# Kernel tuning notes

Hardware: AMD Instinct MI355X
Metric: run time of the kernel (lower is better)

The kernel has to match this reference:

```python
import jax, jax.numpy as jnp
import numpy as np

NEG_SLOPE = 0.2

def edge_softmax(logits, dst, num_nodes):
    # logits: [E, H]; softmax over incoming edges of each dst node, per head
    m = jax.ops.segment_max(logits, dst, num_segments=num_nodes)  # [N, H]
    e = jnp.exp(logits - m[dst])
    s = jax.ops.segment_sum(e, dst, num_segments=num_nodes)  # [N, H]
    return e / s[dst]

def gat_layer(h, src, dst, W, al, ar, b, activation):
    # W: [F_in, H*D], al/ar: [H, D], b: [H, D]
    N = h.shape[0]
    H, D = al.shape
    feat = (h @ W).reshape(N, H, D)
    el = jnp.sum(feat * al, axis=-1)  # [N, H]
    er = jnp.sum(feat * ar, axis=-1)  # [N, H]
    e = jax.nn.leaky_relu(el[src] + er[dst], NEG_SLOPE)  # [E, H]
    a = edge_softmax(e, dst, N)  # [E, H]
    msg = feat[src] * a[:, :, None]  # [E, H, D]
    rst = jax.ops.segment_sum(msg, dst, num_segments=N) + b[None]  # [N, H, D]
    if activation:
        rst = jax.nn.relu(rst)
    return rst

def setup_inputs() -> dict:
    key = jax.random.key(0)
    ks = jax.random.split(key, 16)
    N, E = 50000, 800000
    IN, HID, OUT, H = 128, 64, 64, 4
    s = 0.1
    return {
        "features": jax.random.normal(ks[0], (N, IN), jnp.float32),
        "src": jax.random.randint(ks[1], (E,), 0, N),
        "dst": jax.random.randint(ks[2], (E,), 0, N),
        "W1": jax.random.normal(ks[3], (IN, H * HID), jnp.float32) * s,
        "al1": jax.random.normal(ks[4], (H, HID), jnp.float32) * s,
        "ar1": jax.random.normal(ks[5], (H, HID), jnp.float32) * s,
        "b1": jnp.zeros((H, HID), jnp.float32),
        "W2": jax.random.normal(ks[6], (H * HID, H * HID), jnp.float32) * s,
        "al2": jax.random.normal(ks[7], (H, HID), jnp.float32) * s,
        "ar2": jax.random.normal(ks[8], (H, HID), jnp.float32) * s,
        "b2": jnp.zeros((H, HID), jnp.float32),
        "W3": jax.random.normal(ks[9], (H * HID, OUT), jnp.float32) * s,
        "al3": jax.random.normal(ks[10], (1, OUT), jnp.float32) * s,
        "ar3": jax.random.normal(ks[11], (1, OUT), jnp.float32) * s,
        "b3": jnp.zeros((1, OUT), jnp.float32),
    }

def reference(features, src, dst, W1, al1, ar1, b1, W2, al2, ar2, b2, W3, al3, ar3, b3):
    N = features.shape[0]
    h = gat_layer(features, src, dst, W1, al1, ar1, b1, activation=True)   # [N, 4, 64]
    h = h.reshape(N, -1)                                                    # [N, 256]
    h = gat_layer(h, src, dst, W2, al2, ar2, b2, activation=True)          # [N, 4, 64]
    h = h.reshape(N, -1)                                                    # [N, 256]
    h = gat_layer(h, src, dst, W3, al3, ar3, b3, activation=False)         # [N, 1, 64]
    return h.mean(axis=1)                                                   # [N, 64]
```

## Files before the change

kernel.cpp:

```cpp
#include <hip/hip_runtime.h>
#include <hip/hip_bf16.h>

#define LEAKY 0.2f

typedef __attribute__((ext_vector_type(8))) short short8;
typedef __attribute__((ext_vector_type(4))) float f32x4;

__device__ inline unsigned short f2b(float f) {
    unsigned u = __float_as_uint(f);
    u += 0x7FFFu + ((u >> 16) & 1u);
    return (unsigned short)(u >> 16);
}
__device__ inline float b2f(unsigned short s) {
    return __uint_as_float(((unsigned)s) << 16);
}

#define NEB 8192


__global__ __launch_bounds__(256)
void k_prep(const float* __restrict__ features, unsigned short* __restrict__ fconv,
            int n4,
            const float* __restrict__ W1, const float* __restrict__ W2,
            const float* __restrict__ W3, unsigned short* __restrict__ Wt1,
            unsigned short* __restrict__ Wt2, unsigned short* __restrict__ Wt3,
            const int* __restrict__ dst, int* __restrict__ hist, int nbb,
            int E, int N) {
    __shared__ int lc[256];
    const int tid = threadIdx.x;
    if (blockIdx.x < nbb) {
        lc[tid] = 0;
        __syncthreads();
        const int b0 = blockIdx.x * NEB;
        const int cnt = min(NEB, E - b0);
        for (int j = 0; j < NEB / 256; ++j) {
            int idx = j * 256 + tid;
            if (idx < cnt) {
                int dn = dst[b0 + idx];
                if ((unsigned)dn < (unsigned)N) atomicAdd(&lc[dn >> 8], 1);
            }
        }
        __syncthreads();
        hist[blockIdx.x * 256 + tid] = lc[tid];
        return;
    }
    int idx = (blockIdx.x - nbb) * 256 + tid;
    if (idx < n4) {
        float4 v = *(const float4*)(features + idx * 4);
        ushort4 o;
        o.x = f2b(v.x); o.y = f2b(v.y); o.z = f2b(v.z); o.w = f2b(v.w);
        *(ushort4*)(fconv + idx * 4) = o;
        return;
    }
    int j = idx - n4;
    if (j < 32768) {
        int m = j >> 7, k = j & 127;
        Wt1[j] = f2b(W1[(size_t)k * 256 + m]);
        return;
    }
    if (j < 98304) {
        int jj = j - 32768;
        int m = jj >> 8, k = jj & 255;
        Wt2[jj] = f2b(W2[(size_t)k * 256 + m]);
        return;
    }
    if (j < 114688) {
        int jj = j - 98304;
        int m = jj >> 8, k = jj & 255;
        Wt3[jj] = f2b(W3[(size_t)k * 64 + m]);
    }
}


__global__ __launch_bounds__(256)
void k_bucket_scan(const int* __restrict__ hist, int nbb, int* __restrict__ bbase,
                   int* __restrict__ bcur, int* __restrict__ row_start_N, int B, int E) {
    __shared__ int ws[4];
    const int tid = threadIdx.x, lane = tid & 63, wave = tid >> 6;
    int v = 0;
    for (int blk = 0; blk < nbb; ++blk) v += hist[blk * 256 + tid];
    if (tid >= B) v = 0;
    int x = v;
    #pragma unroll
    for (int off = 1; off < 64; off <<= 1) {
        int t = __shfl_up(x, off, 64);
        if (lane >= off) x += t;
    }
    if (lane == 63) ws[wave] = x;
    __syncthreads();
    if (tid == 0) {
        int c = 0;
        #pragma unroll
        for (int wv = 0; wv < 4; ++wv) { int t = ws[wv]; ws[wv] = c; c += t; }
    }
    __syncthreads();
    int excl = x - v + ws[wave];
    if (tid < B) { bbase[tid] = excl; bcur[tid] = excl; }
    if (tid == 0) { bbase[B] = E; *row_start_N = E; }
}

__global__ __launch_bounds__(256)
void k_bin_scatter(const int* __restrict__ dst, int* __restrict__ bcur,
                   int* __restrict__ ebuf, int E, int N) {
    __shared__ int lc[256], lofs[256], lcur[256], gres[256];
    __shared__ int stage_e[NEB];
    __shared__ unsigned short stage_d[NEB];
    __shared__ int ws[4];
    const int tid = threadIdx.x, lane = tid & 63, wave = tid >> 6;
    const int b0 = blockIdx.x * NEB;
    const int cnt = min(NEB, E - b0);
    lc[tid] = 0;
    __syncthreads();

    int dreg[NEB / 256];
    #pragma unroll
    for (int j = 0; j < NEB / 256; ++j) {
        int idx = j * 256 + tid;
        dreg[j] = -1;
        if (idx < cnt) {
            int dn = dst[b0 + idx];
            if ((unsigned)dn < (unsigned)N) {
                dreg[j] = dn;
                atomicAdd(&lc[dn >> 8], 1);
            }
        }
    }
    __syncthreads();
    {
        int v = lc[tid];
        int x = v;
        #pragma unroll
        for (int off = 1; off < 64; off <<= 1) {
            int t = __shfl_up(x, off, 64);
            if (lane >= off) x += t;
        }
        if (lane == 63) ws[wave] = x;
        __syncthreads();
        if (tid == 0) {
            int c = 0;
            #pragma unroll
            for (int wv = 0; wv < 4; ++wv) { int t = ws[wv]; ws[wv] = c; c += t; }
        }
        __syncthreads();
        int excl = x - v + ws[wave];
        lofs[tid] = excl;
        lcur[tid] = excl;
    }
    __syncthreads();
    #pragma unroll
    for (int j = 0; j < NEB / 256; ++j) {
        int dn = dreg[j];
        if (dn >= 0) {
            int p = atomicAdd(&lcur[dn >> 8], 1);
            stage_e[p] = b0 + j * 256 + tid;
            stage_d[p] = (unsigned short)dn;
        }
    }
    __syncthreads();
    if (lc[tid] > 0) gres[tid] = atomicAdd(&bcur[tid], lc[tid]);
    __syncthreads();
    int total = lcur[255];
    for (int i = tid; i < total; i += 256) {
        int dn = stage_d[i];
        int k = dn >> 8;
        int dest = gres[k] + (i - lofs[k]);
        ebuf[dest] = ((dn & 255) << 24) | stage_e[i];
    }
}

__global__ __launch_bounds__(256)
void k_csr_build(const int* __restrict__ ebuf, const int* __restrict__ src,
                 const int* __restrict__ bbase, int* __restrict__ row_start,
                 int* __restrict__ src_sorted, int N) {
    __shared__ int lc[256], lcur[256];
    __shared__ int ws[4];
    const int tid = threadIdx.x, lane = tid & 63, wave = tid >> 6;
    const int k = blockIdx.x;
    const int base = k << 8;
    const int e0 = bbase[k];
    const int cnt = bbase[k + 1] - e0;
    lc[tid] = 0;
    __syncthreads();
    for (int i = tid; i < cnt; i += 256) {
        int rel = ((unsigned)ebuf[e0 + i]) >> 24;
        atomicAdd(&lc[rel], 1);
    }
    __syncthreads();
    {
        int v = lc[tid];
        int x = v;
        #pragma unroll
        for (int off = 1; off < 64; off <<= 1) {
            int t = __shfl_up(x, off, 64);
            if (lane >= off) x += t;
        }
        if (lane == 63) ws[wave] = x;
        __syncthreads();
        if (tid == 0) {
            int c = 0;
            #pragma unroll
            for (int wv = 0; wv < 4; ++wv) { int t = ws[wv]; ws[wv] = c; c += t; }
        }
        __syncthreads();
        int excl = x - v + ws[wave];
        lcur[tid] = excl;
        int n = base + tid;
        if (n < N) row_start[n] = e0 + excl;
    }
    __syncthreads();
    for (int i = tid; i < cnt; i += 256) {
        int val = ebuf[e0 + i];
        int rel = ((unsigned)val) >> 24;
        int e = val & 0xFFFFFF;
        int p = atomicAdd(&lcur[rel], 1);
        src_sorted[e0 + p] = src[e];
    }
}


__global__ __launch_bounds__(256)
void k_gemm_mfma(const unsigned short* __restrict__ A, const unsigned short* __restrict__ Wt,
                 unsigned short* __restrict__ Cb, const float* __restrict__ al,
                 const float* __restrict__ ar, float* __restrict__ el,
                 float* __restrict__ er, int N, int K, int M) {
    constexpr int STR = 40;
    __shared__ unsigned short As[128 * STR];
    __shared__ unsigned short Bs[128 * STR];
    const int tid  = threadIdx.x;
    const int wave = tid >> 6;
    const int lane = tid & 63;
    const int row0 = blockIdx.y * 128;
    const int col0 = blockIdx.x * 128;
    const int wr = (wave >> 1) * 64;
    const int wc = (wave & 1) * 64;
    const int m16 = lane & 15;
    const int q   = lane >> 4;

    const int s_row = tid >> 1;
    const int s_off = (tid & 1) * 16;

    f32x4 acc[4][4] = {};

    for (int k0 = 0; k0 < K; k0 += 32) {
        {
            int gr = row0 + s_row;
            short8 z = {};
            short8 v0 = z, v1 = z;
            if (gr < N) {
                const unsigned short* ap = A + (size_t)gr * K + k0 + s_off;
                v0 = *(const short8*)ap;
                v1 = *(const short8*)(ap + 8);
            }
            *(short8*)&As[s_row * STR + s_off]     = v0;
            *(short8*)&As[s_row * STR + s_off + 8] = v1;
        }
        {
            const unsigned short* sp = Wt + (size_t)(col0 + s_row) * K + k0 + s_off;
            *(short8*)&Bs[s_row * STR + s_off]     = *(const short8*)sp;
            *(short8*)&Bs[s_row * STR + s_off + 8] = *(const short8*)(sp + 8);
        }
        __syncthreads();

        short8 afr[4], bfr[4];
        #pragma unroll
        for (int rg = 0; rg < 4; ++rg)
            afr[rg] = *(const short8*)&As[(wr + rg * 16 + m16) * STR + q * 8];
        #pragma unroll
        for (int cg = 0; cg < 4; ++cg)
            bfr[cg] = *(const short8*)&Bs[(wc + cg * 16 + m16) * STR + q * 8];
        #pragma unroll
        for (int rg = 0; rg < 4; ++rg)
            #pragma unroll
            for (int cg = 0; cg < 4; ++cg)
                acc[rg][cg] = __builtin_amdgcn_mfma_f32_16x16x32_bf16(
                    afr[rg], bfr[cg], acc[rg][cg], 0, 0, 0);
        __syncthreads();
    }

    const int H = M >> 6;
    const int h = (col0 + wc) >> 6;
    float alv[4], arv[4];
    #pragma unroll
    for (int cg = 0; cg < 4; ++cg) {
        alv[cg] = al[h * 64 + cg * 16 + m16];
        arv[cg] = ar[h * 64 + cg * 16 + m16];
    }

    #pragma unroll
    for (int rg = 0; rg < 4; ++rg) {
        #pragma unroll
        for (int r = 0; r < 4; ++r) {
            int gr = row0 + wr + rg * 16 + q * 4 + r;
            float pl = 0.f, pr = 0.f;
            #pragma unroll
            for (int cg = 0; cg < 4; ++cg) {
                pl = fmaf(acc[rg][cg][r], alv[cg], pl);
                pr = fmaf(acc[rg][cg][r], arv[cg], pr);
            }
            #pragma unroll
            for (int off = 1; off < 16; off <<= 1) {
                pl += __shfl_xor(pl, off, 64);
                pr += __shfl_xor(pr, off, 64);
            }
            if (gr < N) {
                unsigned short* bp = Cb + (size_t)gr * M + col0 + wc + m16;
                #pragma unroll
                for (int cg = 0; cg < 4; ++cg)
                    bp[cg * 16] = f2b(acc[rg][cg][r]);
                if (m16 == 0) {
                    el[gr * H + h] = pl;
                    er[gr * H + h] = pr;
                }
            }
        }
    }
}


__global__ __launch_bounds__(256)
void k_gemm_mfma64(const unsigned short* __restrict__ A, const unsigned short* __restrict__ Wt,
                   unsigned short* __restrict__ Cb, const float* __restrict__ al,
                   const float* __restrict__ ar, float* __restrict__ el,
                   float* __restrict__ er, int N, int K) {
    constexpr int M = 64;
    constexpr int STR = 40;
    __shared__ unsigned short As[256 * STR];
    __shared__ unsigned short Bs[64 * STR];
    const int tid  = threadIdx.x;
    const int wave = tid >> 6;
    const int lane = tid & 63;
    const int row0 = blockIdx.x * 256;
    const int wr = wave * 64;
    const int m16 = lane & 15;
    const int q   = lane >> 4;

    const int s_row = tid >> 1;
    const int s_off = (tid & 1) * 16;
    const int b_row = tid >> 2;
    const int b_chk = (tid & 3) * 8;

    f32x4 acc[4][4] = {};

    for (int k0 = 0; k0 < K; k0 += 32) {
        #pragma unroll
        for (int p = 0; p < 2; ++p) {
            int r = s_row + p * 128;
            int gr = row0 + r;
            short8 z = {};
            short8 v0 = z, v1 = z;
            if (gr < N) {
                const unsigned short* ap = A + (size_t)gr * K + k0 + s_off;
                v0 = *(const short8*)ap;
                v1 = *(const short8*)(ap + 8);
            }
            *(short8*)&As[r * STR + s_off]     = v0;
            *(short8*)&As[r * STR + s_off + 8] = v1;
        }
        {
            const unsigned short* sp = Wt + (size_t)b_row * K + k0 + b_chk;
            *(short8*)&Bs[b_row * STR + b_chk] = *(const short8*)sp;
        }
        __syncthreads();

        short8 afr[4], bfr[4];
        #pragma unroll
        for (int rg = 0; rg < 4; ++rg)
            afr[rg] = *(const short8*)&As[(wr + rg * 16 + m16) * STR + q * 8];
        #pragma unroll
        for (int cg = 0; cg < 4; ++cg)
            bfr[cg] = *(const short8*)&Bs[(cg * 16 + m16) * STR + q * 8];
        #pragma unroll
        for (int rg = 0; rg < 4; ++rg)
            #pragma unroll
            for (int cg = 0; cg < 4; ++cg)
                acc[rg][cg] = __builtin_amdgcn_mfma_f32_16x16x32_bf16(
                    afr[rg], bfr[cg], acc[rg][cg], 0, 0, 0);
        __syncthreads();
    }

    float alv[4], arv[4];
    #pragma unroll
    for (int cg = 0; cg < 4; ++cg) {
        alv[cg] = al[cg * 16 + m16];
        arv[cg] = ar[cg * 16 + m16];
    }

    #pragma unroll
    for (int rg = 0; rg < 4; ++rg) {
        #pragma unroll
        for (int r = 0; r < 4; ++r) {
            int gr = row0 + wr + rg * 16 + q * 4 + r;
            float pl = 0.f, pr = 0.f;
            #pragma unroll
            for (int cg = 0; cg < 4; ++cg) {
                pl = fmaf(acc[rg][cg][r], alv[cg], pl);
                pr = fmaf(acc[rg][cg][r], arv[cg], pr);
            }
            #pragma unroll
            for (int off = 1; off < 16; off <<= 1) {
                pl += __shfl_xor(pl, off, 64);
                pr += __shfl_xor(pr, off, 64);
            }
            if (gr < N) {
                unsigned short* bp = Cb + (size_t)gr * M + m16;
                #pragma unroll
                for (int cg = 0; cg < 4; ++cg)
                    bp[cg * 16] = f2b(acc[rg][cg][r]);
                if (m16 == 0) {
                    el[gr] = pl;
                    er[gr] = pr;
                }
            }
        }
    }
}

template<int OUTBF>
__global__ __launch_bounds__(256)
void k_agg_f(const int* __restrict__ row_start, const int* __restrict__ src_sorted,
             const uint4* __restrict__ featp, const float* __restrict__ el,
             const float* __restrict__ er, const float* __restrict__ bias,
             void* __restrict__ outv, int H, int N, int do_relu) {
    const int M = H * 64;
    const int P = M >> 3;
    const int G = 256 / P;
    const int grp = threadIdx.x / P;
    const int t = threadIdx.x - grp * P;
    const int n = blockIdx.x * G + grp;
    if (n >= N) return;
    const int d0 = t * 8;
    const int h = d0 >> 6;
    const float erv = er[n * H + h];

    const int b0 = row_start[n], b1 = row_start[n + 1];

    float a[8] = {};
    float sum = 0.f;
    int i = b0;
    for (; i + 8 <= b1; i += 8) {
        int ss[8]; float wv[8]; uint4 pv[8];
        #pragma unroll
        for (int j = 0; j < 8; ++j) ss[j] = src_sorted[i + j];
        #pragma unroll
        for (int j = 0; j < 8; ++j) wv[j] = el[(size_t)ss[j] * H + h];
        #pragma unroll
        for (int j = 0; j < 8; ++j) pv[j] = featp[(size_t)ss[j] * P + t];
        #pragma unroll
        for (int j = 0; j < 8; ++j) {
            float x = wv[j] + erv;
            x = (x > 0.f) ? x : LEAKY * x;
            float w = __expf(x);
            wv[j] = w;
            sum += w;
        }
        #pragma unroll
        for (int j = 0; j < 8; ++j) {
            a[0] = fmaf(__uint_as_float(pv[j].x << 16),         wv[j], a[0]);
            a[1] = fmaf(__uint_as_float(pv[j].x & 0xFFFF0000u), wv[j], a[1]);
            a[2] = fmaf(__uint_as_float(pv[j].y << 16),         wv[j], a[2]);
            a[3] = fmaf(__uint_as_float(pv[j].y & 0xFFFF0000u), wv[j], a[3]);
            a[4] = fmaf(__uint_as_float(pv[j].z << 16),         wv[j], a[4]);
            a[5] = fmaf(__uint_as_float(pv[j].z & 0xFFFF0000u), wv[j], a[5]);
            a[6] = fmaf(__uint_as_float(pv[j].w << 16),         wv[j], a[6]);
            a[7] = fmaf(__uint_as_float(pv[j].w & 0xFFFF0000u), wv[j], a[7]);
        }
    }
    for (; i + 4 <= b1; i += 4) {
        int ss[4]; float wv[4]; uint4 pv[4];
        #pragma unroll
        for (int j = 0; j < 4; ++j) ss[j] = src_sorted[i + j];
        #pragma unroll
        for (int j = 0; j < 4; ++j) wv[j] = el[(size_t)ss[j] * H + h];
        #pragma unroll
        for (int j = 0; j < 4; ++j) pv[j] = featp[(size_t)ss[j] * P + t];
        #pragma unroll
        for (int j = 0; j < 4; ++j) {
            float x = wv[j] + erv;
            x = (x > 0.f) ? x : LEAKY * x;
            float w = __expf(x);
            wv[j] = w;
            sum += w;
        }
        #pragma unroll
        for (int j = 0; j < 4; ++j) {
            a[0] = fmaf(__uint_as_float(pv[j].x << 16),         wv[j], a[0]);
            a[1] = fmaf(__uint_as_float(pv[j].x & 0xFFFF0000u), wv[j], a[1]);
            a[2] = fmaf(__uint_as_float(pv[j].y << 16),         wv[j], a[2]);
            a[3] = fmaf(__uint_as_float(pv[j].y & 0xFFFF0000u), wv[j], a[3]);
            a[4] = fmaf(__uint_as_float(pv[j].z << 16),         wv[j], a[4]);
            a[5] = fmaf(__uint_as_float(pv[j].z & 0xFFFF0000u), wv[j], a[5]);
            a[6] = fmaf(__uint_as_float(pv[j].w << 16),         wv[j], a[6]);
            a[7] = fmaf(__uint_as_float(pv[j].w & 0xFFFF0000u), wv[j], a[7]);
        }
    }
    for (; i < b1; ++i) {
        int ss = src_sorted[i];
        float x = el[(size_t)ss * H + h] + erv;
        uint4 pv = featp[(size_t)ss * P + t];
        x = (x > 0.f) ? x : LEAKY * x;
        float w = __expf(x);
        sum += w;
        a[0] = fmaf(__uint_as_float(pv.x << 16),         w, a[0]);
        a[1] = fmaf(__uint_as_float(pv.x & 0xFFFF0000u), w, a[1]);
        a[2] = fmaf(__uint_as_float(pv.y << 16),         w, a[2]);
        a[3] = fmaf(__uint_as_float(pv.y & 0xFFFF0000u), w, a[3]);
        a[4] = fmaf(__uint_as_float(pv.z << 16),         w, a[4]);
        a[5] = fmaf(__uint_as_float(pv.z & 0xFFFF0000u), w, a[5]);
        a[6] = fmaf(__uint_as_float(pv.w << 16),         w, a[6]);
        a[7] = fmaf(__uint_as_float(pv.w & 0xFFFF0000u), w, a[7]);
    }

    float rs = 1.0f / fmaxf(sum, 1e-30f);
    float4 bv0 = *(const float4*)(bias + d0);
    float4 bv1 = *(const float4*)(bias + d0 + 4);
    a[0] = fmaf(a[0], rs, bv0.x); a[1] = fmaf(a[1], rs, bv0.y);
    a[2] = fmaf(a[2], rs, bv0.z); a[3] = fmaf(a[3], rs, bv0.w);
    a[4] = fmaf(a[4], rs, bv1.x); a[5] = fmaf(a[5], rs, bv1.y);
    a[6] = fmaf(a[6], rs, bv1.z); a[7] = fmaf(a[7], rs, bv1.w);
    if (do_relu) {
        #pragma unroll
        for (int j = 0; j < 8; ++j) a[j] = fmaxf(a[j], 0.f);
    }
    if (OUTBF) {
        uint4 o;
        o.x = (unsigned)f2b(a[0]) | ((unsigned)f2b(a[1]) << 16);
        o.y = (unsigned)f2b(a[2]) | ((unsigned)f2b(a[3]) << 16);
        o.z = (unsigned)f2b(a[4]) | ((unsigned)f2b(a[5]) << 16);
        o.w = (unsigned)f2b(a[6]) | ((unsigned)f2b(a[7]) << 16);
        *(uint4*)((unsigned short*)outv + (size_t)n * M + d0) = o;
    } else {
        *(float4*)((float*)outv + (size_t)n * M + d0)     = make_float4(a[0], a[1], a[2], a[3]);
        *(float4*)((float*)outv + (size_t)n * M + d0 + 4) = make_float4(a[4], a[5], a[6], a[7]);
    }
}


static void run_layer(const unsigned short* A, int K, const unsigned short* Wt,
                      const float* al_, const float* ar_, const float* b_, int H,
                      unsigned short* featb, void* rstOut, bool outBf,
                      float* el, float* er,
                      const int* row_start, const int* src_sorted,
                      int N, int E, bool do_relu, hipStream_t stream) {
    const int M = H * 64;
    if (M % 128 == 0) {
        dim3 gg(M / 128, (N + 127) / 128);
        k_gemm_mfma<<<gg, 256, 0, stream>>>(A, Wt, featb, al_, ar_, el, er, N, K, M);
    } else {
        k_gemm_mfma64<<<(N + 255) / 256, 256, 0, stream>>>(A, Wt, featb, al_, ar_, el, er, N, K);
    }

    int G = 256 / (M / 8);
    if (outBf)
        k_agg_f<1><<<(N + G - 1) / G, 256, 0, stream>>>(row_start, src_sorted,
                                                        (const uint4*)featb, el, er,
                                                        b_, rstOut, H, N, do_relu ? 1 : 0);
    else
        k_agg_f<0><<<(N + G - 1) / G, 256, 0, stream>>>(row_start, src_sorted,
                                                        (const uint4*)featb, el, er,
                                                        b_, rstOut, H, N, do_relu ? 1 : 0);
}

extern "C" void kernel_launch(void* const* d_in, const int* in_sizes, int n_in,
                              void* d_out, int out_size, void* d_ws, size_t ws_size,
                              hipStream_t stream) {
    const float* features = (const float*)d_in[0];
    const int*   src = (const int*)d_in[1];
    const int*   dst = (const int*)d_in[2];
    const float* W1  = (const float*)d_in[3];
    const float* al1 = (const float*)d_in[4];
    const float* ar1 = (const float*)d_in[5];
    const float* b1  = (const float*)d_in[6];
    const float* W2  = (const float*)d_in[7];
    const float* al2 = (const float*)d_in[8];
    const float* ar2 = (const float*)d_in[9];
    const float* b2  = (const float*)d_in[10];
    const float* W3  = (const float*)d_in[11];
    const float* al3 = (const float*)d_in[12];
    const float* ar3 = (const float*)d_in[13];
    const float* b3  = (const float*)d_in[14];

    const int N = in_sizes[0] / 128;
    const int E = in_sizes[1];
    const int B = (N + 255) >> 8;
    const int n4 = N * 128 / 4;
    const int nbb = (E + NEB - 1) / NEB;

    float* ws   = (float*)d_ws;
    float* el   = ws;
    float* er   = el + (size_t)N * 4;
    int* row_start  = (int*)(er + (size_t)N * 4);
    int* src_sorted = row_start + N + 1;
    int* ebuf       = src_sorted + E;
    int* bbase      = ebuf + E;
    int* bcur       = bbase + 257;
    int* hist       = bcur + 256;
    uintptr_t wp = (uintptr_t)(hist + (size_t)nbb * 256);
    wp = (wp + 15) & ~(uintptr_t)15;
    unsigned short* Wt1   = (unsigned short*)wp;
    unsigned short* Wt2   = Wt1 + 32768;
    unsigned short* Wt3   = Wt2 + 65536;
    unsigned short* fconv = Wt3 + 16384;
    unsigned short* featb = fconv + (size_t)N * 128;
    unsigned short* rstb  = featb + (size_t)N * 256;

    int prep_total = n4 + 114688;
    int prep_blocks = nbb + (prep_total + 255) / 256;
    k_prep<<<prep_blocks, 256, 0, stream>>>(features, fconv, n4,
                                            W1, W2, W3, Wt1, Wt2, Wt3,
                                            dst, hist, nbb, E, N);

    k_bucket_scan<<<1, 256, 0, stream>>>(hist, nbb, bbase, bcur, row_start + N, B, E);
    k_bin_scatter<<<nbb, 256, 0, stream>>>(dst, bcur, ebuf, E, N);
    k_csr_build<<<B, 256, 0, stream>>>(ebuf, src, bbase, row_start, src_sorted, N);

    run_layer(fconv, 128, Wt1, al1, ar1, b1, 4, featb, rstb, true,
              el, er, row_start, src_sorted, N, E, true, stream);
    run_layer(rstb, 256, Wt2, al2, ar2, b2, 4, featb, rstb, true,
              el, er, row_start, src_sorted, N, E, true, stream);
    run_layer(rstb, 256, Wt3, al3, ar3, b3, 1, featb, d_out, false,
              el, er, row_start, src_sorted, N, E, false, stream);
}
```

Measured before the change: 398.1 us.

## Double-buffer edge gathers in aggregation, use exp2 with pre-scaled logits, template head count

The aggregation kernel's main edge loop now software-pipelines batches of eight edges. It issues the next batch's index, logit and feature gathers before computing on the current batch, to hide gather latency. The GEMM epilogues pre-multiply el/er by log2(e) so the softmax weight can use the hardware exp2 instruction directly, and leaky-relu becomes a max. The head count is a template parameter and indices use 32-bit arithmetic, which cuts address math. Holding two buffers in flight raises register pressure and may reduce occupancy.

```diff
diff --git a/kernel.cpp b/kernel.cpp
--- a/kernel.cpp
+++ b/kernel.cpp
@@ -2,6 +2,7 @@
 #include <hip/hip_bf16.h>
 
 #define LEAKY 0.2f
+#define LOG2E 1.44269504f
 
 typedef __attribute__((ext_vector_type(8))) short short8;
 typedef __attribute__((ext_vector_type(4))) float f32x4;
@@ -14,6 +15,7 @@
 __device__ inline float b2f(unsigned short s) {
     return __uint_as_float(((unsigned)s) << 16);
 }
+__device__ inline float fexp2(float x) { return __builtin_amdgcn_exp2f(x); }
 
 #define NEB 8192
 
@@ -308,8 +310,8 @@
                 for (int cg = 0; cg < 4; ++cg)
                     bp[cg * 16] = f2b(acc[rg][cg][r]);
                 if (m16 == 0) {
-                    el[gr * H + h] = pl;
-                    er[gr * H + h] = pr;
+                    el[gr * H + h] = pl * LOG2E;
+                    er[gr * H + h] = pr * LOG2E;
                 }
             }
         }
@@ -407,77 +409,102 @@
                 for (int cg = 0; cg < 4; ++cg)
                     bp[cg * 16] = f2b(acc[rg][cg][r]);
                 if (m16 == 0) {
-                    el[gr] = pl;
-                    er[gr] = pr;
+                    el[gr] = pl * LOG2E;
+                    er[gr] = pr * LOG2E;
                 }
             }
         }
     }
 }
 
-template<int OUTBF>
+
+#define AGG_LOADB(SS, ELV, PV, BASE) do {                                     \
+    _Pragma("unroll") for (int j = 0; j < 8; ++j)                             \
+        SS[j] = src_sorted[(BASE) + j];                                       \
+    _Pragma("unroll") for (int j = 0; j < 8; ++j)                             \
+        ELV[j] = el[(unsigned)(SS[j] * HH + h)];                              \
+    _Pragma("unroll") for (int j = 0; j < 8; ++j)                             \
+        PV[j] = featp[(unsigned)(SS[j] * P + t)];                             \
+} while (0)
+
+#define AGG_COMPUTEB(ELV, PV) do {                                            \
+    float wvv[8];                                                             \
+    _Pragma("unroll") for (int j = 0; j < 8; ++j) {                           \
+        float x = ELV[j] + erv;                                               \
+        x = fmaxf(x, LEAKY * x);                                              \
+        float w = fexp2(x);                                                   \
+        wvv[j] = w; sum += w;                                                 \
+    }                                                                         \
+    _Pragma("unroll") for (int j = 0; j < 8; ++j) {                           \
+        a[0] = fmaf(__uint_as_float(PV[j].x << 16),         wvv[j], a[0]);    \
+        a[1] = fmaf(__uint_as_float(PV[j].x & 0xFFFF0000u), wvv[j], a[1]);    \
+        a[2] = fmaf(__uint_as_float(PV[j].y << 16),         wvv[j], a[2]);    \
+        a[3] = fmaf(__uint_as_float(PV[j].y & 0xFFFF0000u), wvv[j], a[3]);    \
+        a[4] = fmaf(__uint_as_float(PV[j].z << 16),         wvv[j], a[4]);    \
+        a[5] = fmaf(__uint_as_float(PV[j].z & 0xFFFF0000u), wvv[j], a[5]);    \
+        a[6] = fmaf(__uint_as_float(PV[j].w << 16),         wvv[j], a[6]);    \
+        a[7] = fmaf(__uint_as_float(PV[j].w & 0xFFFF0000u), wvv[j], a[7]);    \
+    }                                                                         \
+} while (0)
+
+template<int OUTBF, int HH>
 __global__ __launch_bounds__(256)
 void k_agg_f(const int* __restrict__ row_start, const int* __restrict__ src_sorted,
              const uint4* __restrict__ featp, const float* __restrict__ el,
              const float* __restrict__ er, const float* __restrict__ bias,
-             void* __restrict__ outv, int H, int N, int do_relu) {
-    const int M = H * 64;
-    const int P = M >> 3;
-    const int G = 256 / P;
+             void* __restrict__ outv, int N, int do_relu) {
+    constexpr int M = HH * 64;
+    constexpr int P = M >> 3;
+    constexpr int G = 256 / P;
     const int grp = threadIdx.x / P;
     const int t = threadIdx.x - grp * P;
     const int n = blockIdx.x * G + grp;
     if (n >= N) return;
     const int d0 = t * 8;
     const int h = d0 >> 6;
-    const float erv = er[n * H + h];
+    const float erv = er[n * HH + h];
 
     const int b0 = row_start[n], b1 = row_start[n + 1];
 
     float a[8] = {};
     float sum = 0.f;
-    int i = b0;
-    for (; i + 8 <= b1; i += 8) {
-        int ss[8]; float wv[8]; uint4 pv[8];
-        #pragma unroll
-        for (int j = 0; j < 8; ++j) ss[j] = src_sorted[i + j];
-        #pragma unroll
-        for (int j = 0; j < 8; ++j) wv[j] = el[(size_t)ss[j] * H + h];
-        #pragma unroll
-        for (int j = 0; j < 8; ++j) pv[j] = featp[(size_t)ss[j] * P + t];
-        #pragma unroll
-        for (int j = 0; j < 8; ++j) {
-            float x = wv[j] + erv;
-            x = (x > 0.f) ? x : LEAKY * x;
-            float w = __expf(x);
-            wv[j] = w;
-            sum += w;
-        }
-        #pragma unroll
-        for (int j = 0; j < 8; ++j) {
-            a[0] = fmaf(__uint_as_float(pv[j].x << 16),         wv[j], a[0]);
-            a[1] = fmaf(__uint_as_float(pv[j].x & 0xFFFF0000u), wv[j], a[1]);
-            a[2] = fmaf(__uint_as_float(pv[j].y << 16),         wv[j], a[2]);
-            a[3] = fmaf(__uint_as_float(pv[j].y & 0xFFFF0000u), wv[j], a[3]);
-            a[4] = fmaf(__uint_as_float(pv[j].z << 16),         wv[j], a[4]);
-            a[5] = fmaf(__uint_as_float(pv[j].z & 0xFFFF0000u), wv[j], a[5]);
-            a[6] = fmaf(__uint_as_float(pv[j].w << 16),         wv[j], a[6]);
-            a[7] = fmaf(__uint_as_float(pv[j].w & 0xFFFF0000u), wv[j], a[7]);
-        }
-    }
+
+    const int nb = (b1 - b0) >> 3;
+    if (nb > 0) {
+        int   ssA[8], ssB[8];
+        float elA[8], elB[8];
+        uint4 pvA[8], pvB[8];
+        AGG_LOADB(ssA, elA, pvA, b0);
+        int b = 0;
+        for (; b + 2 < nb; b += 2) {
+            AGG_LOADB(ssB, elB, pvB, b0 + (b + 1) * 8);
+            AGG_COMPUTEB(elA, pvA);
+            AGG_LOADB(ssA, elA, pvA, b0 + (b + 2) * 8);
+            AGG_COMPUTEB(elB, pvB);
+        }
+        if (b + 1 < nb) {
+            AGG_LOADB(ssB, elB, pvB, b0 + (b + 1) * 8);
+            AGG_COMPUTEB(elA, pvA);
+            AGG_COMPUTEB(elB, pvB);
+        } else {
+            AGG_COMPUTEB(elA, pvA);
+        }
+    }
+
+    int i = b0 + nb * 8;
     for (; i + 4 <= b1; i += 4) {
         int ss[4]; float wv[4]; uint4 pv[4];
         #pragma unroll
         for (int j = 0; j < 4; ++j) ss[j] = src_sorted[i + j];
         #pragma unroll
-        for (int j = 0; j < 4; ++j) wv[j] = el[(size_t)ss[j] * H + h];
-        #pragma unroll
-        for (int j = 0; j < 4; ++j) pv[j] = featp[(size_t)ss[j] * P + t];
+        for (int j = 0; j < 4; ++j) wv[j] = el[(unsigned)(ss[j] * HH + h)];
+        #pragma unroll
+        for (int j = 0; j < 4; ++j) pv[j] = featp[(unsigned)(ss[j] * P + t)];
         #pragma unroll
         for (int j = 0; j < 4; ++j) {
             float x = wv[j] + erv;
-            x = (x > 0.f) ? x : LEAKY * x;
-            float w = __expf(x);
+            x = fmaxf(x, LEAKY * x);
+            float w = fexp2(x);
             wv[j] = w;
             sum += w;
         }
@@ -495,10 +522,10 @@
     }
     for (; i < b1; ++i) {
         int ss = src_sorted[i];
-        float x = el[(size_t)ss * H + h] + erv;
-        uint4 pv = featp[(size_t)ss * P + t];
-        x = (x > 0.f) ? x : LEAKY * x;
-        float w = __expf(x);
+        float x = el[(unsigned)(ss * HH + h)] + erv;
+        uint4 pv = featp[(unsigned)(ss * P + t)];
+        x = fmaxf(x, LEAKY * x);
+        float w = fexp2(x);
         sum += w;
         a[0] = fmaf(__uint_as_float(pv.x << 16),         w, a[0]);
         a[1] = fmaf(__uint_as_float(pv.x & 0xFFFF0000u), w, a[1]);
@@ -550,14 +577,26 @@
     }
 
     int G = 256 / (M / 8);
-    if (outBf)
-        k_agg_f<1><<<(N + G - 1) / G, 256, 0, stream>>>(row_start, src_sorted,
-                                                        (const uint4*)featb, el, er,
-                                                        b_, rstOut, H, N, do_relu ? 1 : 0);
-    else
-        k_agg_f<0><<<(N + G - 1) / G, 256, 0, stream>>>(row_start, src_sorted,
-                                                        (const uint4*)featb, el, er,
-                                                        b_, rstOut, H, N, do_relu ? 1 : 0);
+    int blocks = (N + G - 1) / G;
+    if (H == 4) {
+        if (outBf)
+            k_agg_f<1, 4><<<blocks, 256, 0, stream>>>(row_start, src_sorted,
+                                                      (const uint4*)featb, el, er,
+                                                      b_, rstOut, N, do_relu ? 1 : 0);
+        else
+            k_agg_f<0, 4><<<blocks, 256, 0, stream>>>(row_start, src_sorted,
+                                                      (const uint4*)featb, el, er,
+                                                      b_, rstOut, N, do_relu ? 1 : 0);
+    } else {
+        if (outBf)
+            k_agg_f<1, 1><<<blocks, 256, 0, stream>>>(row_start, src_sorted,
+                                                      (const uint4*)featb, el, er,
+                                                      b_, rstOut, N, do_relu ? 1 : 0);
+        else
+            k_agg_f<0, 1><<<blocks, 256, 0, stream>>>(row_start, src_sorted,
+                                                      (const uint4*)featb, el, er,
+                                                      b_, rstOut, N, do_relu ? 1 : 0);
+    }
 }
 
 extern "C" void kernel_launch(void* const* d_in, const int* in_sizes, int n_in,
```

Measured after the change: 404.5 us. No clear change (+1.6%).
